# Performance work log

Measured on AMD Instinct MI355X. Metric: run time of the kernel, lower is better.

Reference implementation:

```python
import jax, jax.numpy as jnp
import numpy as np
import math

B, L, D = 2, 2048, 1024
H = 16
DH = D // H


def setup_inputs() -> dict:
    key = jax.random.key(0)
    k1, k2, k3, k4 = jax.random.split(key, 4)
    s = 1.0 / math.sqrt(D)
    return {
        "x": jax.random.normal(k1, (B, L, D), dtype=jnp.float32),
        "w_in": jax.random.normal(k2, (3 * D, D), dtype=jnp.float32) * s,
        "b_in": jax.random.normal(k3, (3 * D,), dtype=jnp.float32) * 0.01,
        "w_out": jax.random.normal(k4, (D, D), dtype=jnp.float32) * s,
        "causal_mask": 1,
    }


def reference(x, w_in, b_in, w_out, causal_mask):
    b, seq_len, d = x.shape
    # fused QKV projection: (B,L,3D)
    qkv = x @ w_in.T + b_in
    q, k, v = jnp.split(qkv, 3, axis=-1)
    # (B,L,D) -> (B,H,L,DH)
    def heads(t):
        return t.reshape(b, seq_len, H, DH).transpose(0, 2, 1, 3)
    q, k, v = heads(q), heads(k), heads(v)
    scores = jnp.einsum("bhqd,bhkd->bhqk", q, k) / math.sqrt(DH)
    if causal_mask:
        causal = jnp.triu(jnp.ones((seq_len, seq_len), dtype=bool), k=1)
        scores = jnp.where(causal[None, None, :, :], jnp.float32(-1e9), scores)
    # stable softmax (amax-subtract as in original)
    weight = jax.nn.softmax(scores, axis=-1)
    out = jnp.einsum("bhqk,bhkd->bhqd", weight, v)
    out = out.transpose(0, 2, 1, 3).reshape(b, seq_len, d)
    return out @ w_out.T
```

## Files before the change

### kernel.cpp

```cpp
#include <hip/hip_runtime.h>
#include <hip/hip_bf16.h>

typedef __attribute__((ext_vector_type(8))) short short8;
typedef __attribute__((ext_vector_type(4))) short short4v;
typedef __attribute__((ext_vector_type(4))) float f32x4;
typedef __attribute__((ext_vector_type(2))) unsigned uint2v;

#define BB 2
#define LL 2048
#define DD 1024
#define HH 16
#define DHH 64
#define KK 1024
#define SCL 0.18033688011112042f
#define EXP2(x) __builtin_amdgcn_exp2f(x)

__device__ __forceinline__ void gload_lds16(const void* g, void* l) {
  __builtin_amdgcn_global_load_lds((const __attribute__((address_space(1))) void*)g,
                                   (__attribute__((address_space(3))) void*)l,
                                   16, 0, 0);
}

__device__ __forceinline__ unsigned short f2b(float x) {
  __hip_bfloat16 h = __float2bfloat16(x);
  return *reinterpret_cast<unsigned short*>(&h);
}

__device__ __forceinline__ unsigned cvtpk(float lo, float hi) {
  unsigned r;
  asm("v_cvt_pk_bf16_f32 %0, %1, %2" : "=v"(r) : "v"(lo), "v"(hi));
  return r;
}

#define NX8  ((BB * LL * DD) / 8)
#define NWI8 ((3 * DD * DD) / 8)
#define NWO8 ((DD * DD) / 8)
__global__ void cvt_all(const float* __restrict__ x,
                        const float* __restrict__ w_in,
                        const float* __restrict__ w_out,
                        __hip_bfloat16* __restrict__ xb,
                        __hip_bfloat16* __restrict__ w_inb,
                        __hip_bfloat16* __restrict__ w_outb) {
  int i = blockIdx.x * blockDim.x + threadIdx.x;
  const float* src;
  __hip_bfloat16* dst;
  int j;
  if (i < NX8)              { src = x;     dst = xb;     j = i; }
  else if (i < NX8 + NWI8)  { src = w_in;  dst = w_inb;  j = i - NX8; }
  else                      { src = w_out; dst = w_outb; j = i - NX8 - NWI8; }
  const f32x4 a = ((const f32x4*)src)[j * 2];
  const f32x4 b = ((const f32x4*)src)[j * 2 + 1];
  short8 o;
#pragma unroll
  for (int k = 0; k < 4; ++k) o[k] = (short)f2b(a[k]);
#pragma unroll
  for (int k = 0; k < 4; ++k) o[4 + k] = (short)f2b(b[k]);
  ((short8*)dst)[j] = o;
}

template<bool QKV>
__global__ void gemm_bt(const __hip_bfloat16* __restrict__ A,
                        const __hip_bfloat16* __restrict__ Bm,
                        const float* __restrict__ bias,
                        __hip_bfloat16* __restrict__ Cq,
                        __hip_bfloat16* __restrict__ Ck,
                        __hip_bfloat16* __restrict__ Cv,
                        float* __restrict__ Cd,
                        int N, int nbn) {
  __shared__ __align__(16) char As[16384];
  __shared__ __align__(16) char Bs[16384];
  const int tid = threadIdx.x;
  const int lane = tid & 63, wid = tid >> 6;
  const int l15 = lane & 15, lhi = lane >> 4;
  const int wm = wid >> 1, wn = wid & 1;
  const int bn = blockIdx.x % nbn, bm = blockIdx.x / nbn;
  const int m0 = bm * 128, n0 = bn * 128;

  f32x4 acc[4][4] = {};

  for (int kt = 0; kt < KK / 64; ++kt) {
    const int k0 = kt * 64;
    __syncthreads();
#pragma unroll
    for (int j = 0; j < 4; ++j) {
      int c = wid * 256 + j * 64 + lane;
      int row = c >> 3;
      int ab = ((c & 7) * 16) ^ ((row & 7) << 4);
      gload_lds16(A + (size_t)(m0 + row) * KK + k0 + (ab >> 1),
                  As + wid * 4096 + j * 1024);
    }
#pragma unroll
    for (int j = 0; j < 4; ++j) {
      int c = wid * 256 + j * 64 + lane;
      int row = c >> 3;
      int ab = ((c & 7) * 16) ^ ((row & 7) << 4);
      gload_lds16(Bm + (size_t)(n0 + row) * KK + k0 + (ab >> 1),
                  Bs + wid * 4096 + j * 1024);
    }
    __syncthreads();

#pragma unroll
    for (int kk = 0; kk < 2; ++kk) {
      short8 af[4], bf[4];
#pragma unroll
      for (int mf = 0; mf < 4; ++mf) {
        int row = wm * 64 + mf * 16 + l15;
        int byt = (kk * 64 + lhi * 16) ^ ((row & 7) << 4);
        af[mf] = *(const short8*)(As + row * 128 + byt);
      }
#pragma unroll
      for (int nf = 0; nf < 4; ++nf) {
        int row = wn * 64 + nf * 16 + l15;
        int byt = (kk * 64 + lhi * 16) ^ ((row & 7) << 4);
        bf[nf] = *(const short8*)(Bs + row * 128 + byt);
      }
#pragma unroll
      for (int mf = 0; mf < 4; ++mf)
#pragma unroll
        for (int nf = 0; nf < 4; ++nf)
          acc[mf][nf] = __builtin_amdgcn_mfma_f32_16x16x32_bf16(af[mf], bf[nf],
                                                                acc[mf][nf], 0, 0, 0);
    }
  }

#pragma unroll
  for (int mf = 0; mf < 4; ++mf) {
#pragma unroll
    for (int nf = 0; nf < 4; ++nf) {
      const int n = n0 + wn * 64 + nf * 16 + l15;
      if constexpr (QKV) {
        const int sect = n >> 10;
        const int nn = n & 1023;
        const int h = nn >> 6, dh = nn & 63;
        const float bv = bias[n];
        const int m_base = m0 + wm * 64 + mf * 16 + lhi * 4;
        const int b = m_base >> 11, ml = m_base & 2047;
        if (sect == 2) {
          short4v v;
#pragma unroll
          for (int r = 0; r < 4; ++r) v[r] = (short)f2b(acc[mf][nf][r] + bv);
          *(short4v*)&Cv[(((size_t)(b * HH + h)) * DHH + dh) * LL + ml] = v;
        } else {
          __hip_bfloat16* dst = (sect == 0) ? Cq : Ck;
          const float scl = (sect == 0) ? SCL : 1.0f;
#pragma unroll
          for (int r = 0; r < 4; ++r)
            dst[(((size_t)(b * HH + h)) * LL + ml + r) * DHH + dh] =
                __float2bfloat16((acc[mf][nf][r] + bv) * scl);
        }
      } else {
#pragma unroll
        for (int r = 0; r < 4; ++r) {
          const int m = m0 + wm * 64 + mf * 16 + lhi * 4 + r;
          Cd[(size_t)m * N + n] = acc[mf][nf][r];
        }
      }
    }
  }
}

__global__ __launch_bounds__(128)
__attribute__((amdgpu_waves_per_eu(1, 4)))
void attn_fwd(
    const __hip_bfloat16* __restrict__ Q,
    const __hip_bfloat16* __restrict__ K,
    const __hip_bfloat16* __restrict__ VT,
    __hip_bfloat16* __restrict__ att,
    const int* __restrict__ maskp) {
  __shared__ __align__(16) char shm[8960];
  char* Pw = shm + (threadIdx.x >> 6) * 4096;
  float (*Ob)[68] = (float(*)[68])shm;
  float* Mb = (float*)(shm + 8704);
  float* Lb = (float*)(shm + 8832);
  const int tid = threadIdx.x;
  const int lane = tid & 63, wid = tid >> 6;
  const int l15 = lane & 15, lhi = lane >> 4;
  const int bid = blockIdx.x;
  const int strip = 63 - (bid >> 5);
  const int bh = bid & 31;
  const int causal = *maskp;
  const int r0 = strip * 32;
  const __hip_bfloat16* Qg = Q + (size_t)bh * LL * DHH;
  const __hip_bfloat16* Kg = K + (size_t)bh * LL * DHH;
  const __hip_bfloat16* VTg = VT + (size_t)bh * DHH * LL;
  const int swz = (l15 & 7) << 4;

  short8 aq[2][2];
#pragma unroll
  for (int mf = 0; mf < 2; ++mf)
#pragma unroll
    for (int ks = 0; ks < 2; ++ks)
      aq[mf][ks] = *(const short8*)(Qg + (size_t)(r0 + mf * 16 + l15) * DHH +
                                    ks * 32 + lhi * 8);

  f32x4 o[2][4] = {};
  float mrun[2] = {-1e30f, -1e30f};
  float lrun[2] = {0.0f, 0.0f};

  const int nt = causal ? ((r0 + 31) >> 6) + 1 : (LL / 64);
  const int hf = (nt + 1) >> 1;
  const int t0 = wid ? hf : 0;
  const int t1 = wid ? nt : hf;

  const __hip_bfloat16* kb0 = Kg + (size_t)(t0 * 64 + l15) * DHH + lhi * 8;
  const __hip_bfloat16* kb2 = Kg + (size_t)(t0 * 64 + 32 + l15) * DHH + lhi * 8;
  const __hip_bfloat16* vp0 = VTg + (size_t)(l15) * LL + t0 * 64 + lhi * 8;
  const __hip_bfloat16* vp1 = VTg + (size_t)(16 + l15) * LL + t0 * 64 + lhi * 8;
  const __hip_bfloat16* vp2 = VTg + (size_t)(32 + l15) * LL + t0 * 64 + lhi * 8;
  const __hip_bfloat16* vp3 = VTg + (size_t)(48 + l15) * LL + t0 * 64 + lhi * 8;

  for (int t = t0; t < t1; ++t) {
    const int kv0 = t * 64;
    f32x4 s[2][4] = {};

    short8 kah[4];
    kah[0] = *(const short8*)(kb0);
    kah[1] = *(const short8*)(kb0 + 1024);
    kah[2] = *(const short8*)(kb2);
    kah[3] = *(const short8*)(kb2 + 1024);
    short8 bv[4][2];
    bv[0][0] = *(const short8*)(vp0);  bv[0][1] = *(const short8*)(vp0 + 32);
    bv[1][0] = *(const short8*)(vp1);  bv[1][1] = *(const short8*)(vp1 + 32);
    bv[2][0] = *(const short8*)(vp2);  bv[2][1] = *(const short8*)(vp2 + 32);
    bv[3][0] = *(const short8*)(vp3);  bv[3][1] = *(const short8*)(vp3 + 32);

    __builtin_amdgcn_s_setprio(1);
#pragma unroll
    for (int nf = 0; nf < 4; ++nf) {
      s[0][nf] = __builtin_amdgcn_mfma_f32_16x16x32_bf16(kah[nf], aq[0][0], s[0][nf], 0, 0, 0);
      s[1][nf] = __builtin_amdgcn_mfma_f32_16x16x32_bf16(kah[nf], aq[1][0], s[1][nf], 0, 0, 0);
    }
    __builtin_amdgcn_s_setprio(0);
    kah[0] = *(const short8*)(kb0 + 32);
    kah[1] = *(const short8*)(kb0 + 1024 + 32);
    kah[2] = *(const short8*)(kb2 + 32);
    kah[3] = *(const short8*)(kb2 + 1024 + 32);
    __builtin_amdgcn_s_setprio(1);
#pragma unroll
    for (int nf = 0; nf < 4; ++nf) {
      s[0][nf] = __builtin_amdgcn_mfma_f32_16x16x32_bf16(kah[nf], aq[0][1], s[0][nf], 0, 0, 0);
      s[1][nf] = __builtin_amdgcn_mfma_f32_16x16x32_bf16(kah[nf], aq[1][1], s[1][nf], 0, 0, 0);
    }
    __builtin_amdgcn_s_setprio(0);

    kb0 += 4096; kb2 += 4096;
    vp0 += 64; vp1 += 64; vp2 += 64; vp3 += 64;

    const bool needmask = causal && (kv0 + 63 > r0);
#pragma unroll
    for (int mf = 0; mf < 2; ++mf) {
      const int q = r0 + mf * 16 + l15;
      if (needmask)
#pragma unroll
        for (int nf = 0; nf < 4; ++nf) {
          const int kvb = kv0 + nf * 16 + lhi * 4;
#pragma unroll
          for (int r = 0; r < 4; ++r)
            if (kvb + r > q) s[mf][nf][r] = -1e30f;
        }
      f32x4 t4 = s[mf][0];
#pragma unroll
      for (int nf = 1; nf < 4; ++nf)
#pragma unroll
        for (int r = 0; r < 4; ++r) t4[r] = fmaxf(t4[r], s[mf][nf][r]);
      float pm = fmaxf(fmaxf(t4[0], t4[1]), fmaxf(t4[2], t4[3]));
      pm = fmaxf(pm, __shfl_xor(pm, 16, 64));
      pm = fmaxf(pm, __shfl_xor(pm, 32, 64));
      if (__any(pm > mrun[mf] + 8.0f)) {
        const float mnew = fmaxf(mrun[mf], pm);
        const float sc = EXP2(mrun[mf] - mnew);
        mrun[mf] = mnew;
        lrun[mf] *= sc;
#pragma unroll
        for (int nf = 0; nf < 4; ++nf)
#pragma unroll
          for (int r = 0; r < 4; ++r) o[mf][nf][r] *= sc;
      }
      float rs = 0.0f;
#pragma unroll
      for (int nf = 0; nf < 4; ++nf)
#pragma unroll
        for (int r = 0; r < 4; ++r) {
          float p = EXP2(s[mf][nf][r] - mrun[mf]);
          s[mf][nf][r] = p;
          rs += p;
        }
      rs += __shfl_xor(rs, 16, 64);
      rs += __shfl_xor(rs, 32, 64);
      lrun[mf] += rs;

      char* base = Pw + (mf * 16 + l15) * 128;
#pragma unroll
      for (int nf = 0; nf < 4; ++nf) {
        unsigned lo = cvtpk(s[mf][nf][0], s[mf][nf][1]);
        unsigned hi = cvtpk(s[mf][nf][2], s[mf][nf][3]);
        *(unsigned long long*)(base + ((nf * 32 + lhi * 8) ^ swz)) =
            (unsigned long long)lo | ((unsigned long long)hi << 32);
      }
    }

    __builtin_amdgcn_s_setprio(1);
#pragma unroll
    for (int mf = 0; mf < 2; ++mf) {
      const char* base = Pw + (mf * 16 + l15) * 128;
      short8 ap0 = *(const short8*)(base + ((lhi * 16) ^ swz));
      short8 ap1 = *(const short8*)(base + ((64 + lhi * 16) ^ swz));
#pragma unroll
      for (int nf = 0; nf < 4; ++nf) {
        o[mf][nf] = __builtin_amdgcn_mfma_f32_16x16x32_bf16(bv[nf][0], ap0, o[mf][nf], 0, 0, 0);
        o[mf][nf] = __builtin_amdgcn_mfma_f32_16x16x32_bf16(bv[nf][1], ap1, o[mf][nf], 0, 0, 0);
      }
    }
    __builtin_amdgcn_s_setprio(0);
  }

  __syncthreads();
  if (wid == 1) {
#pragma unroll
    for (int mf = 0; mf < 2; ++mf) {
      const int row = mf * 16 + l15;
      if (lhi == 0) { Mb[row] = mrun[mf]; Lb[row] = lrun[mf]; }
#pragma unroll
      for (int nf = 0; nf < 4; ++nf)
        *(f32x4*)&Ob[row][nf * 16 + lhi * 4] = o[mf][nf];
    }
  }
  __syncthreads();
  if (wid == 0) {
    const int b_ = bh >> 4, h = bh & 15;
#pragma unroll
    for (int mf = 0; mf < 2; ++mf) {
      const int row = mf * 16 + l15;
      const float m1 = Mb[row], l1 = Lb[row];
      const float mt = fmaxf(mrun[mf], m1);
      const float sc0 = EXP2(mrun[mf] - mt);
      const float sc1 = EXP2(m1 - mt);
      const float inv = 1.0f / (lrun[mf] * sc0 + l1 * sc1);
      __hip_bfloat16* dst = att + ((size_t)(b_ * LL + r0 + row)) * DD + h * DHH;
#pragma unroll
      for (int nf = 0; nf < 4; ++nf) {
        f32x4 ov = *(const f32x4*)&Ob[row][nf * 16 + lhi * 4];
        float f0 = (o[mf][nf][0] * sc0 + ov[0] * sc1) * inv;
        float f1 = (o[mf][nf][1] * sc0 + ov[1] * sc1) * inv;
        float f2 = (o[mf][nf][2] * sc0 + ov[2] * sc1) * inv;
        float f3 = (o[mf][nf][3] * sc0 + ov[3] * sc1) * inv;
        uint2v pk;
        pk[0] = cvtpk(f0, f1);
        pk[1] = cvtpk(f2, f3);
        *(uint2v*)(dst + nf * 16 + lhi * 4) = pk;
      }
    }
  }
}

extern "C" void kernel_launch(void* const* d_in, const int* in_sizes, int n_in,
                              void* d_out, int out_size, void* d_ws, size_t ws_size,
                              hipStream_t stream) {
  const float* x     = (const float*)d_in[0];
  const float* w_in  = (const float*)d_in[1];
  const float* b_in  = (const float*)d_in[2];
  const float* w_out = (const float*)d_in[3];
  const int* mask    = (const int*)d_in[4];
  float* out = (float*)d_out;

  char* ws = (char*)d_ws;
  const size_t MiB = 1024u * 1024u;
  __hip_bfloat16* xb    = (__hip_bfloat16*)(ws);
  __hip_bfloat16* w_inb = (__hip_bfloat16*)(ws + 8 * MiB);
  __hip_bfloat16* w_outb= (__hip_bfloat16*)(ws + 14 * MiB);
  __hip_bfloat16* Qb    = (__hip_bfloat16*)(ws + 16 * MiB);
  __hip_bfloat16* Kb    = (__hip_bfloat16*)(ws + 24 * MiB);
  __hip_bfloat16* Vtb   = (__hip_bfloat16*)(ws + 32 * MiB);
  __hip_bfloat16* att   = (__hip_bfloat16*)(ws + 40 * MiB);

  cvt_all<<<dim3(4096), dim3(256), 0, stream>>>(x, w_in, w_out, xb, w_inb, w_outb);

  gemm_bt<true><<<dim3(32 * 24), dim3(256), 0, stream>>>(
      xb, w_inb, b_in, Qb, Kb, Vtb, nullptr, 3072, 24);
  attn_fwd<<<dim3(2048), dim3(128), 0, stream>>>(Qb, Kb, Vtb, att, mask);
  gemm_bt<false><<<dim3(32 * 8), dim3(256), 0, stream>>>(
      att, w_outb, nullptr, nullptr, nullptr, nullptr, out, 1024, 8);
}
```

Measured before the change: 129.8 us.

## Split attention KV range across four waves with tree merge

Result: slower. 138.3 us (+6.5%).

```diff
diff --git a/kernel.cpp b/kernel.cpp
--- a/kernel.cpp
+++ b/kernel.cpp
@@ -159,7 +159,7 @@
   }
 }
 
-__global__ __launch_bounds__(128)
+__global__ __launch_bounds__(256)
 __attribute__((amdgpu_waves_per_eu(1, 4)))
 void attn_fwd(
     const __hip_bfloat16* __restrict__ Q,
@@ -167,11 +167,11 @@
     const __hip_bfloat16* __restrict__ VT,
     __hip_bfloat16* __restrict__ att,
     const int* __restrict__ maskp) {
-  __shared__ __align__(16) char shm[8960];
+  __shared__ __align__(16) char shm[17920];
   char* Pw = shm + (threadIdx.x >> 6) * 4096;
-  float (*Ob)[68] = (float(*)[68])shm;
-  float* Mb = (float*)(shm + 8704);
-  float* Lb = (float*)(shm + 8832);
+  float (*Ob)[32][68] = (float(*)[32][68])shm;
+  float (*Mb)[32] = (float(*)[32])(shm + 17408);
+  float (*Lb)[32] = (float(*)[32])(shm + 17664);
   const int tid = threadIdx.x;
   const int lane = tid & 63, wid = tid >> 6;
   const int l15 = lane & 15, lhi = lane >> 4;
@@ -198,9 +198,8 @@
   float lrun[2] = {0.0f, 0.0f};
 
   const int nt = causal ? ((r0 + 31) >> 6) + 1 : (LL / 64);
-  const int hf = (nt + 1) >> 1;
-  const int t0 = wid ? hf : 0;
-  const int t1 = wid ? nt : hf;
+  const int t0 = (wid * nt) >> 2;
+  const int t1 = ((wid + 1) * nt) >> 2;
 
   const __hip_bfloat16* kb0 = Kg + (size_t)(t0 * 64 + l15) * DHH + lhi * 8;
   const __hip_bfloat16* kb2 = Kg + (size_t)(t0 * 64 + 32 + l15) * DHH + lhi * 8;
@@ -314,39 +313,56 @@
     __builtin_amdgcn_s_setprio(0);
   }
 
+  auto dump = [&](int b) {
+#pragma unroll
+    for (int mf = 0; mf < 2; ++mf) {
+      const int row = mf * 16 + l15;
+      if (lhi == 0) { Mb[b][row] = mrun[mf]; Lb[b][row] = lrun[mf]; }
+#pragma unroll
+      for (int nf = 0; nf < 4; ++nf)
+        *(f32x4*)&Ob[b][row][nf * 16 + lhi * 4] = o[mf][nf];
+    }
+  };
+  auto combine = [&](int b) {
+#pragma unroll
+    for (int mf = 0; mf < 2; ++mf) {
+      const int row = mf * 16 + l15;
+      const float mo = Mb[b][row], lo = Lb[b][row];
+      const float mt = fmaxf(mrun[mf], mo);
+      const float sr = EXP2(mrun[mf] - mt);
+      const float so = EXP2(mo - mt);
+      lrun[mf] = lrun[mf] * sr + lo * so;
+      mrun[mf] = mt;
+#pragma unroll
+      for (int nf = 0; nf < 4; ++nf) {
+        f32x4 ov = *(const f32x4*)&Ob[b][row][nf * 16 + lhi * 4];
+#pragma unroll
+        for (int r = 0; r < 4; ++r)
+          o[mf][nf][r] = o[mf][nf][r] * sr + ov[r] * so;
+      }
+    }
+  };
+
   __syncthreads();
-  if (wid == 1) {
-#pragma unroll
-    for (int mf = 0; mf < 2; ++mf) {
-      const int row = mf * 16 + l15;
-      if (lhi == 0) { Mb[row] = mrun[mf]; Lb[row] = lrun[mf]; }
-#pragma unroll
-      for (int nf = 0; nf < 4; ++nf)
-        *(f32x4*)&Ob[row][nf * 16 + lhi * 4] = o[mf][nf];
-    }
-  }
+  if (wid & 1) dump(wid >> 1);
+  __syncthreads();
+  if (!(wid & 1)) combine(wid >> 1);
+  __syncthreads();
+  if (wid == 2) dump(0);
   __syncthreads();
   if (wid == 0) {
+    combine(0);
     const int b_ = bh >> 4, h = bh & 15;
 #pragma unroll
     for (int mf = 0; mf < 2; ++mf) {
       const int row = mf * 16 + l15;
-      const float m1 = Mb[row], l1 = Lb[row];
-      const float mt = fmaxf(mrun[mf], m1);
-      const float sc0 = EXP2(mrun[mf] - mt);
-      const float sc1 = EXP2(m1 - mt);
-      const float inv = 1.0f / (lrun[mf] * sc0 + l1 * sc1);
+      const float inv = 1.0f / lrun[mf];
       __hip_bfloat16* dst = att + ((size_t)(b_ * LL + r0 + row)) * DD + h * DHH;
 #pragma unroll
       for (int nf = 0; nf < 4; ++nf) {
-        f32x4 ov = *(const f32x4*)&Ob[row][nf * 16 + lhi * 4];
-        float f0 = (o[mf][nf][0] * sc0 + ov[0] * sc1) * inv;
-        float f1 = (o[mf][nf][1] * sc0 + ov[1] * sc1) * inv;
-        float f2 = (o[mf][nf][2] * sc0 + ov[2] * sc1) * inv;
-        float f3 = (o[mf][nf][3] * sc0 + ov[3] * sc1) * inv;
         uint2v pk;
-        pk[0] = cvtpk(f0, f1);
-        pk[1] = cvtpk(f2, f3);
+        pk[0] = cvtpk(o[mf][nf][0] * inv, o[mf][nf][1] * inv);
+        pk[1] = cvtpk(o[mf][nf][2] * inv, o[mf][nf][3] * inv);
         *(uint2v*)(dst + nf * 16 + lhi * 4) = pk;
       }
     }
@@ -377,7 +393,7 @@
 
   gemm_bt<true><<<dim3(32 * 24), dim3(256), 0, stream>>>(
       xb, w_inb, b_in, Qb, Kb, Vtb, nullptr, 3072, 24);
-  attn_fwd<<<dim3(2048), dim3(128), 0, stream>>>(Qb, Kb, Vtb, att, mask);
+  attn_fwd<<<dim3(2048), dim3(256), 0, stream>>>(Qb, Kb, Vtb, att, mask);
   gemm_bt<false><<<dim3(32 * 8), dim3(256), 0, stream>>>(
       att, w_outb, nullptr, nullptr, nullptr, nullptr, out, 1024, 8);
 }
```
